# Performance work log

Hardware: AMD Instinct MI355X
Metric: run time of the kernel (lower is better)

Reference implementation:

```python
import jax, jax.numpy as jnp
import numpy as np

B, S, H = 256, 196, 1024  # batch, image_size**2, hidden_size


def _linear_init(key, fan_in, fan_out):
    kw, kb = jax.random.split(key)
    lim = 1.0 / np.sqrt(fan_in)
    W = jax.random.uniform(kw, (fan_in, fan_out), jnp.float32, -lim, lim)
    b = jax.random.uniform(kb, (fan_out,), jnp.float32, -lim, lim)
    return W, b


def setup_inputs() -> dict:
    key = jax.random.key(0)
    ks = jax.random.split(key, 7)
    v = jax.random.normal(ks[0], (B, S, H), jnp.float32)
    h = jax.random.normal(ks[1], (B, H), jnp.float32)
    W_fc, b_fc = _linear_init(ks[2], H, 2 * H)
    W_v, b_v = _linear_init(ks[3], H, H)
    W_h, b_h = _linear_init(ks[4], H, H)
    W_s, b_s = _linear_init(ks[5], H, H)
    W_z, b_z = _linear_init(ks[6], H, 1)
    return {"v": v, "h": h, "W_fc": W_fc, "b_fc": b_fc, "W_v": W_v, "b_v": b_v,
            "W_h": W_h, "b_h": b_h, "W_s": W_s, "b_s": b_s, "W_z": W_z, "b_z": b_z}


def reference(v, h, W_fc, b_fc, W_v, b_v, W_h, b_h, W_s, b_s, W_z, b_z):
    # Dropout is identity in eval mode.
    hs = jnp.tanh(h[:, None, :] @ W_fc + b_fc)          # (B, 1, 2H)
    h1, s = hs[..., :H], hs[..., H:]                    # each (B, 1, H)
    _v = v @ W_v + b_v                                  # (B, S, H)
    _h = h1 @ W_h + b_h                                 # (B, 1, H)
    _s = s @ W_s + b_s                                  # (B, 1, H)
    z = jnp.tanh(jnp.concatenate([_v, _s], axis=1) + _h)  # (B, S+1, H)
    z = (z @ W_z + b_z)[..., 0]                         # (B, S+1)
    a = jax.nn.softmax(z, axis=1)                       # (B, S+1)
    vc = jnp.concatenate([v, s], axis=1)                # (B, S+1, H)
    c = jnp.sum(a[:, :, None] * vc, axis=1)             # (B, H)
    return a, c
```

## Files before the change

### kernel.cpp

```cpp
#include <hip/hip_runtime.h>
#include <hip/hip_bf16.h>
#include <cstdint>
#include <cstddef>

#define Bb  256
#define Ss  196
#define Hh  1024
#define SP1 197
#define Mm  50176

typedef float  f32x4 __attribute__((ext_vector_type(4)));
typedef short  s16x8 __attribute__((ext_vector_type(8)));
typedef unsigned short u16;
typedef unsigned short u16x8 __attribute__((ext_vector_type(8)));

__device__ __forceinline__ u16 f2b(float f) {
  __hip_bfloat16 b = __float2bfloat16(f);
  u16 r; __builtin_memcpy(&r, &b, 2); return r;
}
__device__ __forceinline__ float b2f(u16 u) {
  return __uint_as_float(((unsigned)u) << 16);
}
__device__ __forceinline__ float ftanh(float x) {
  float ax = fabsf(x);
  float t = __expf(-2.f * ax);
  float r = (1.f - t) * __builtin_amdgcn_rcpf(1.f + t);
  return copysignf(r, x);
}
__device__ __forceinline__ void gload16(const u16* g, u16* l) {
  __builtin_amdgcn_global_load_lds(
      (const __attribute__((address_space(1))) unsigned int*)(const void*)g,
      (__attribute__((address_space(3))) unsigned int*)(void*)l, 16, 0, 0);
}

__device__ __forceinline__ void cvtV_core(int bid, const float* __restrict__ V,
                                          u16* __restrict__ Vb) {
  for (int c = bid * 256 + (int)threadIdx.x; c < Mm * 128; c += 2048 * 256) {
    int m = c >> 7;
    int k8 = (c & 127) << 3;
    f32x4 a = *(const f32x4*)(V + (size_t)m * Hh + k8);
    f32x4 b = *(const f32x4*)(V + (size_t)m * Hh + k8 + 4);
    u16x8 w;
    w[0] = f2b(a.x); w[1] = f2b(a.y); w[2] = f2b(a.z); w[3] = f2b(a.w);
    w[4] = f2b(b.x); w[5] = f2b(b.y); w[6] = f2b(b.z); w[7] = f2b(b.w);
    *(u16x8*)(Vb + (size_t)m * Hh + (k8 ^ ((m & 7) << 3))) = w;
  }
}

__device__ __forceinline__ void transpose_core(int bid, float* sm,
                                               const float* __restrict__ Wv,
                                               u16* __restrict__ WvT) {
  float (*t)[65] = (float(*)[65])sm;
  int k0 = (bid & 15) * 64;
  int n0 = (bid >> 4) * 64;
  int tid = threadIdx.x;
#pragma unroll
  for (int i = 0; i < 16; ++i) {
    int idx = i * 256 + tid;
    int r = idx >> 6, c = idx & 63;
    t[r][c] = Wv[(size_t)(k0 + r) * Hh + n0 + c];
  }
  __syncthreads();
#pragma unroll
  for (int i = 0; i < 16; ++i) {
    int idx = i * 256 + tid;
    int r = idx >> 6, c = idx & 63;
    WvT[(size_t)(n0 + r) * Hh + ((k0 + c) ^ ((r & 7) << 3))] = f2b(t[c][r]);
  }
}

__device__ __forceinline__ void small_gemm_core(int bid, int nct, float* sm,
    const float* __restrict__ X, int ldx,
    const float* __restrict__ W, int ldw,
    const float* __restrict__ bias,
    float* __restrict__ Y, int ldy, int act) {
  int tid = threadIdx.x, lane = tid & 63, w = tid >> 6;
  int ct = bid % nct, bt = bid / nct;
  int col = ct * 64 + lane;
  float acc[16];
#pragma unroll
  for (int b = 0; b < 16; ++b) acc[b] = 0.f;
  int xr = lane >> 2, xc = (lane & 3) * 16;
  for (int kc = 0; kc < 4; ++kc) {
    int kb = w * 256 + kc * 64;
#pragma unroll
    for (int q = 0; q < 4; ++q)
      *(f32x4*)&sm[(w * 16 + xr) * 64 + xc + q * 4] =
          *(const f32x4*)&X[(size_t)(bt * 16 + xr) * ldx + kb + xc + q * 4];
    for (int kl = 0; kl < 64; kl += 4) {
      float w0 = W[(size_t)(kb + kl + 0) * ldw + col];
      float w1 = W[(size_t)(kb + kl + 1) * ldw + col];
      float w2 = W[(size_t)(kb + kl + 2) * ldw + col];
      float w3 = W[(size_t)(kb + kl + 3) * ldw + col];
#pragma unroll
      for (int b = 0; b < 16; ++b) {
        f32x4 x = *(const f32x4*)&sm[(w * 16 + b) * 64 + kl];
        acc[b] += x.x * w0 + x.y * w1 + x.z * w2 + x.w * w3;
      }
    }
  }
#pragma unroll
  for (int b = 0; b < 16; ++b) sm[(w * 16 + b) * 64 + lane] = acc[b];
  __syncthreads();
#pragma unroll
  for (int q = 0; q < 4; ++q) {
    int b = w * 4 + q;
    float s = sm[(0 * 16 + b) * 64 + lane] + sm[(1 * 16 + b) * 64 + lane]
            + sm[(2 * 16 + b) * 64 + lane] + sm[(3 * 16 + b) * 64 + lane]
            + bias[col];
    if (act) s = ftanh(s);
    Y[(size_t)(bt * 16 + b) * ldy + col] = s;
  }
}

__global__ __launch_bounds__(256) void k_pre(const float* __restrict__ v,
                                             u16* __restrict__ Vb,
                                             const float* __restrict__ Wv,
                                             u16* __restrict__ WvT,
                                             const float* __restrict__ h,
                                             const float* __restrict__ Wfc,
                                             const float* __restrict__ bfc,
                                             float* __restrict__ hs,
                                             int pre) {
  __shared__ __align__(16) float sm[64 * 65];
  int bid = blockIdx.x;
  if (bid < 2048) {
    if (pre) cvtV_core(bid, v, Vb);
  } else if (bid < 2304) {
    transpose_core(bid - 2048, sm, Wv, WvT);
  } else {
    small_gemm_core(bid - 2304, 32, sm, h, Hh, Wfc, 2048, bfc, hs, 2048, 1);
  }
}

__global__ __launch_bounds__(256) void k_dual(const float* __restrict__ hs,
                                              const float* __restrict__ Wh,
                                              const float* __restrict__ bh,
                                              const float* __restrict__ Ws_,
                                              const float* __restrict__ bs_,
                                              float* __restrict__ hhp,
                                              float* __restrict__ svp) {
  __shared__ __align__(16) float sm[4 * 16 * 64];
  int bid = blockIdx.x;
  int sel = bid >= 256;
  small_gemm_core(bid - (sel << 8), 16, sm,
                  sel ? hs + 1024 : hs, 2048,
                  sel ? Ws_ : Wh, Hh,
                  sel ? bs_ : bh,
                  sel ? svp : hhp, Hh, 0);
}

#define BK 64
template<int PRE>
__global__ __launch_bounds__(256, PRE ? 2 : 3)
void k_big(const float* __restrict__ V, const u16* __restrict__ Vb,
           const u16* __restrict__ WvT, const float* __restrict__ bv,
           const float* __restrict__ hh, const float* __restrict__ Wz,
           float* __restrict__ zpart) {
  constexpr int LDA_ = PRE ? 64 : 72;
  constexpr int NBUF = PRE ? 2 : 1;
  __shared__ __align__(16) u16 As[NBUF][128 * LDA_];
  __shared__ __align__(16) u16 Bs[NBUF][128 * 64];
  __shared__ float wz_s[128], bv_s[128], hh_s[2][128];
  __shared__ float zred[4][64];

  int bid = blockIdx.x;
  int lin = (bid & 7) * 392 + (bid >> 3);
  int mt = lin >> 3, nt = lin & 7;
  int row0 = mt * 128, n0 = nt * 128;

  int tid = threadIdx.x;
  int lane = tid & 63, wid = tid >> 6;
  int wm = wid >> 1, wn = wid & 1;

  int b0 = row0 / Ss;
  int rsplit = (b0 + 1) * Ss - row0;
  int b1 = (rsplit < 128) ? b0 + 1 : b0;
  if (tid < 128) {
    wz_s[tid] = Wz[n0 + tid];
    bv_s[tid] = bv[n0 + tid];
    hh_s[0][tid] = hh[(size_t)b0 * Hh + n0 + tid];
    hh_s[1][tid] = hh[(size_t)b1 * Hh + n0 + tid];
  }

  f32x4 acc[4][4];
  f32x4 zz = {0.f, 0.f, 0.f, 0.f};
#pragma unroll
  for (int m = 0; m < 4; ++m)
#pragma unroll
    for (int n = 0; n < 4; ++n) acc[m][n] = zz;

  int srow = lane >> 3, scol = (lane & 7) * 8;
  int bxor = (lane & 7) << 3;

  auto stage = [&](int kt, int buf) {
    int k0 = kt * BK;
#pragma unroll
    for (int i = 0; i < 4; ++i) {
      int r = wid * 32 + i * 8;
      gload16(WvT + (size_t)(n0 + r + srow) * Hh + k0 + scol, &Bs[buf][r * 64]);
    }
#pragma unroll
    for (int i = 0; i < 4; ++i) {
      int r = wid * 32 + i * 8;
      gload16(Vb + (size_t)(row0 + r + srow) * Hh + k0 + scol, &As[buf][r * 64]);
    }
  };

  int arow = tid >> 3, acol8 = (tid & 7) * 8;
  const float* Ap = V + (size_t)(row0 + arow) * Hh + acol8;
  f32x4 av[8];
  if constexpr (!PRE) {
#pragma unroll
    for (int j = 0; j < 4; ++j) {
      av[2 * j]     = *(const f32x4*)(Ap + (size_t)j * 32 * Hh);
      av[2 * j + 1] = *(const f32x4*)(Ap + (size_t)j * 32 * Hh + 4);
    }
  }

  if constexpr (PRE) {
    stage(0, 0);
    __syncthreads();
  }
  int cur = 0;

  for (int kt = 0; kt < 16; ++kt) {
    if constexpr (PRE) {
      if (kt < 15) stage(kt + 1, cur ^ 1);
    } else {
      int k0 = kt * BK;
      __syncthreads();
#pragma unroll
      for (int i = 0; i < 4; ++i) {
        int r = wid * 32 + i * 8;
        gload16(WvT + (size_t)(n0 + r + srow) * Hh + k0 + scol, &Bs[0][r * 64]);
      }
#pragma unroll
      for (int j = 0; j < 4; ++j) {
        u16x8 w;
        w[0] = f2b(av[2 * j].x);     w[1] = f2b(av[2 * j].y);
        w[2] = f2b(av[2 * j].z);     w[3] = f2b(av[2 * j].w);
        w[4] = f2b(av[2 * j + 1].x); w[5] = f2b(av[2 * j + 1].y);
        w[6] = f2b(av[2 * j + 1].z); w[7] = f2b(av[2 * j + 1].w);
        *(u16x8*)&As[0][(j * 32 + arow) * LDA_ + acol8] = w;
      }
      if (kt < 15) {
#pragma unroll
        for (int j = 0; j < 4; ++j) {
          av[2 * j]     = *(const f32x4*)(Ap + (size_t)j * 32 * Hh + k0 + BK);
          av[2 * j + 1] = *(const f32x4*)(Ap + (size_t)j * 32 * Hh + k0 + BK + 4);
        }
      }
      __syncthreads();
    }
#pragma unroll
    for (int ks = 0; ks < 2; ++ks) {
      int kk = ks * 32 + (lane >> 4) * 8;
      s16x8 afr[4], bfr[4];
#pragma unroll
      for (int m = 0; m < 4; ++m) {
        int r = wm * 64 + m * 16 + (lane & 15);
        afr[m] = *(const s16x8*)&As[cur][r * LDA_ + (PRE ? (kk ^ bxor) : kk)];
      }
#pragma unroll
      for (int n = 0; n < 4; ++n) {
        int r = wn * 64 + n * 16 + (lane & 15);
        bfr[n] = *(const s16x8*)&Bs[cur][r * 64 + (kk ^ bxor)];
      }
#pragma unroll
      for (int m = 0; m < 4; ++m)
#pragma unroll
        for (int n = 0; n < 4; ++n)
          acc[m][n] = __builtin_amdgcn_mfma_f32_16x16x32_bf16(afr[m], bfr[n], acc[m][n], 0, 0, 0);
    }
    if constexpr (PRE) {
      __syncthreads();
      cur ^= 1;
    }
  }

  int cl = lane & 15, rg = lane >> 4;
  float pz[4][4];
#pragma unroll
  for (int m = 0; m < 4; ++m)
#pragma unroll
    for (int j = 0; j < 4; ++j) pz[m][j] = 0.f;
#pragma unroll
  for (int n = 0; n < 4; ++n) {
    int col = wn * 64 + n * 16 + cl;
    float wzv = wz_s[col], bvv = bv_s[col];
    float h0 = hh_s[0][col], h1 = hh_s[1][col];
#pragma unroll
    for (int m = 0; m < 4; ++m)
#pragma unroll
      for (int j = 0; j < 4; ++j) {
        int r = wm * 64 + m * 16 + rg * 4 + j;
        float hv = (r >= rsplit) ? h1 : h0;
        pz[m][j] += wzv * ftanh(acc[m][n][j] + bvv + hv);
      }
  }
#pragma unroll
  for (int m = 0; m < 4; ++m)
#pragma unroll
    for (int j = 0; j < 4; ++j) {
      float vv = pz[m][j];
      vv += __shfl_xor(vv, 1); vv += __shfl_xor(vv, 2);
      vv += __shfl_xor(vv, 4); vv += __shfl_xor(vv, 8);
      pz[m][j] = vv;
    }
  if (cl == 0) {
#pragma unroll
    for (int m = 0; m < 4; ++m)
#pragma unroll
      for (int j = 0; j < 4; ++j)
        zred[wid][m * 16 + rg * 4 + j] = pz[m][j];
  }
  __syncthreads();
  if (tid < 128) {
    int hhalf = tid >> 6, lr = tid & 63;
    zpart[(size_t)nt * Mm + row0 + tid] =
        zred[hhalf * 2][lr] + zred[hhalf * 2 + 1][lr];
  }
}

__global__ __launch_bounds__(256) void k_softmax(const float* __restrict__ zpart,
                                                 const float* __restrict__ sv,
                                                 const float* __restrict__ hhp,
                                                 const float* __restrict__ Wz,
                                                 const float* __restrict__ bz,
                                                 float* __restrict__ outA) {
  int b = blockIdx.x, tid = threadIdx.x;
  int wid = tid >> 6, lane = tid & 63;
  __shared__ float redm[4], reds[4];
  __shared__ float zSsh;
  {
    int j0 = tid * 4;
    f32x4 s4 = *(const f32x4*)&sv[(size_t)b * Hh + j0];
    f32x4 h4 = *(const f32x4*)&hhp[(size_t)b * Hh + j0];
    f32x4 w4 = *(const f32x4*)&Wz[j0];
    float p = w4.x * ftanh(s4.x + h4.x) + w4.y * ftanh(s4.y + h4.y)
            + w4.z * ftanh(s4.z + h4.z) + w4.w * ftanh(s4.w + h4.w);
#pragma unroll
    for (int d = 1; d < 64; d <<= 1) p += __shfl_xor(p, d);
    if (lane == 0) redm[wid] = p;
    __syncthreads();
    if (tid == 0) zSsh = redm[0] + redm[1] + redm[2] + redm[3] + bz[0];
    __syncthreads();
  }
  float z = -1e30f;
  if (tid < Ss) {
    float s = 0.f;
#pragma unroll
    for (int nt = 0; nt < 8; ++nt) s += zpart[(size_t)nt * Mm + (size_t)b * Ss + tid];
    z = s + bz[0];
  } else if (tid == Ss) {
    z = zSsh;
  }
  float m = z;
#pragma unroll
  for (int d = 1; d < 64; d <<= 1) m = fmaxf(m, __shfl_xor(m, d));
  if (lane == 0) redm[wid] = m;
  __syncthreads();
  m = fmaxf(fmaxf(redm[0], redm[1]), fmaxf(redm[2], redm[3]));
  float e = (tid <= Ss) ? expf(z - m) : 0.f;
  float s = e;
#pragma unroll
  for (int d = 1; d < 64; d <<= 1) s += __shfl_xor(s, d);
  if (lane == 0) reds[wid] = s;
  __syncthreads();
  s = reds[0] + reds[1] + reds[2] + reds[3];
  if (tid <= Ss) outA[(size_t)b * SP1 + tid] = e / s;
}

template<int PRE>
__global__ __launch_bounds__(256) void k_ctx(const float* __restrict__ V,
                                             const u16* __restrict__ Vb,
                                             const float* __restrict__ hs,
                                             const float* __restrict__ A,
                                             float* __restrict__ outC) {
  int b = blockIdx.x >> 2;
  int col = (blockIdx.x & 3) * 256 + threadIdx.x;
  __shared__ float a_s[SP1];
  if (threadIdx.x < SP1) a_s[threadIdx.x] = A[(size_t)b * SP1 + threadIdx.x];
  __syncthreads();
  float acc = a_s[Ss] * hs[(size_t)b * 2048 + 1024 + col];
  if constexpr (PRE) {
    size_t m0 = (size_t)b * Ss;
#pragma unroll 4
    for (int t = 0; t < Ss; ++t) {
      size_t m = m0 + t;
      acc += a_s[t] * b2f(Vb[m * Hh + (col ^ (((int)m & 7) << 3))]);
    }
  } else {
    const float* vb = V + (size_t)b * Ss * Hh + col;
#pragma unroll 4
    for (int t = 0; t < Ss; ++t) acc += a_s[t] * vb[(size_t)t * Hh];
  }
  outC[(size_t)b * Hh + col] = acc;
}

extern "C" void kernel_launch(void* const* d_in, const int* in_sizes, int n_in,
                              void* d_out, int out_size, void* d_ws, size_t ws_size,
                              hipStream_t stream) {
  const float* v   = (const float*)d_in[0];
  const float* h   = (const float*)d_in[1];
  const float* Wfc = (const float*)d_in[2];
  const float* bfc = (const float*)d_in[3];
  const float* Wv  = (const float*)d_in[4];
  const float* bv  = (const float*)d_in[5];
  const float* Wh  = (const float*)d_in[6];
  const float* bh  = (const float*)d_in[7];
  const float* Ws  = (const float*)d_in[8];
  const float* bs  = (const float*)d_in[9];
  const float* Wz  = (const float*)d_in[10];
  const float* bz  = (const float*)d_in[11];
  float* out  = (float*)d_out;
  float* outA = out;
  float* outC = out + (size_t)Bb * SP1;

  float* ws  = (float*)d_ws;
  float* hs  = ws;
  float* hh  = hs + 524288;
  float* sv  = hh + 262144;
  float* zp  = sv + 262144;
  u16*  WvT  = (u16*)(zp + 401408);
  u16*  Vb   = (u16*)((char*)(void*)WvT + 2097152);

  bool pre = ws_size >= 110657536ull;

  k_pre<<<2816, 256, 0, stream>>>(v, Vb, Wv, WvT, h, Wfc, bfc, hs, (int)pre);
  k_dual<<<512, 256, 0, stream>>>(hs, Wh, bh, Ws, bs, hh, sv);
  if (pre) k_big<1><<<3136, 256, 0, stream>>>(v, Vb, WvT, bv, hh, Wz, zp);
  else     k_big<0><<<3136, 256, 0, stream>>>(v, Vb, WvT, bv, hh, Wz, zp);
  k_softmax<<<256, 256, 0, stream>>>(zp, sv, hh, Wz, bz, outA);
  if (pre) k_ctx<1><<<1024, 256, 0, stream>>>(v, Vb, hs, outA, outC);
  else     k_ctx<0><<<1024, 256, 0, stream>>>(v, Vb, hs, outA, outC);
}
```

Measured before the change: 311.5 us.

## Move V swizzle into staging loads, drop GEMM double buffer, widen small GEMMs

The V-to-bf16 conversion now writes an unswizzled layout with 16 elements per thread. The XOR swizzle moves into the k_big staging load addresses, which lets k_ctx read contiguous 4-wide bf16 vectors with one block per batch. k_big drops its LDS double buffer to a single buffer with a sync before and after each load, and raises occupancy to 4 blocks per CU. The small GEMMs handle 32 rows per block instead of 16, halving their block counts but doubling register and LDS use per block. The trade is losing load/compute overlap in the main GEMM in exchange for more resident waves.

```diff
diff --git a/kernel.cpp b/kernel.cpp
--- a/kernel.cpp
+++ b/kernel.cpp
@@ -12,6 +12,7 @@
 typedef float  f32x4 __attribute__((ext_vector_type(4)));
 typedef short  s16x8 __attribute__((ext_vector_type(8)));
 typedef unsigned short u16;
+typedef unsigned short u16x4 __attribute__((ext_vector_type(4)));
 typedef unsigned short u16x8 __attribute__((ext_vector_type(8)));
 
 __device__ __forceinline__ u16 f2b(float f) {
@@ -35,15 +36,21 @@
 
 __device__ __forceinline__ void cvtV_core(int bid, const float* __restrict__ V,
                                           u16* __restrict__ Vb) {
-  for (int c = bid * 256 + (int)threadIdx.x; c < Mm * 128; c += 2048 * 256) {
-    int m = c >> 7;
-    int k8 = (c & 127) << 3;
-    f32x4 a = *(const f32x4*)(V + (size_t)m * Hh + k8);
-    f32x4 b = *(const f32x4*)(V + (size_t)m * Hh + k8 + 4);
-    u16x8 w;
-    w[0] = f2b(a.x); w[1] = f2b(a.y); w[2] = f2b(a.z); w[3] = f2b(a.w);
-    w[4] = f2b(b.x); w[5] = f2b(b.y); w[6] = f2b(b.z); w[7] = f2b(b.w);
-    *(u16x8*)(Vb + (size_t)m * Hh + (k8 ^ ((m & 7) << 3))) = w;
+  for (int c = bid * 256 + (int)threadIdx.x; c < Mm * 64; c += 2048 * 256) {
+    int m = c >> 6;
+    int k16 = (c & 63) << 4;
+    const float* src = V + (size_t)m * Hh + k16;
+    f32x4 a = *(const f32x4*)(src);
+    f32x4 b = *(const f32x4*)(src + 4);
+    f32x4 cc = *(const f32x4*)(src + 8);
+    f32x4 d = *(const f32x4*)(src + 12);
+    u16x8 w0, w1;
+    w0[0] = f2b(a.x); w0[1] = f2b(a.y); w0[2] = f2b(a.z); w0[3] = f2b(a.w);
+    w0[4] = f2b(b.x); w0[5] = f2b(b.y); w0[6] = f2b(b.z); w0[7] = f2b(b.w);
+    w1[0] = f2b(cc.x); w1[1] = f2b(cc.y); w1[2] = f2b(cc.z); w1[3] = f2b(cc.w);
+    w1[4] = f2b(d.x); w1[5] = f2b(d.y); w1[6] = f2b(d.z); w1[7] = f2b(d.w);
+    *(u16x8*)(Vb + (size_t)m * Hh + k16) = w0;
+    *(u16x8*)(Vb + (size_t)m * Hh + k16 + 8) = w1;
   }
 }
 
@@ -77,39 +84,39 @@
   int tid = threadIdx.x, lane = tid & 63, w = tid >> 6;
   int ct = bid % nct, bt = bid / nct;
   int col = ct * 64 + lane;
-  float acc[16];
-#pragma unroll
-  for (int b = 0; b < 16; ++b) acc[b] = 0.f;
-  int xr = lane >> 2, xc = (lane & 3) * 16;
+  float acc[32];
+#pragma unroll
+  for (int b = 0; b < 32; ++b) acc[b] = 0.f;
+  int xr = lane >> 1, xc = (lane & 1) * 32;
   for (int kc = 0; kc < 4; ++kc) {
     int kb = w * 256 + kc * 64;
 #pragma unroll
-    for (int q = 0; q < 4; ++q)
-      *(f32x4*)&sm[(w * 16 + xr) * 64 + xc + q * 4] =
-          *(const f32x4*)&X[(size_t)(bt * 16 + xr) * ldx + kb + xc + q * 4];
+    for (int q = 0; q < 8; ++q)
+      *(f32x4*)&sm[(w * 32 + xr) * 64 + xc + q * 4] =
+          *(const f32x4*)&X[(size_t)(bt * 32 + xr) * ldx + kb + xc + q * 4];
     for (int kl = 0; kl < 64; kl += 4) {
       float w0 = W[(size_t)(kb + kl + 0) * ldw + col];
       float w1 = W[(size_t)(kb + kl + 1) * ldw + col];
       float w2 = W[(size_t)(kb + kl + 2) * ldw + col];
       float w3 = W[(size_t)(kb + kl + 3) * ldw + col];
 #pragma unroll
-      for (int b = 0; b < 16; ++b) {
-        f32x4 x = *(const f32x4*)&sm[(w * 16 + b) * 64 + kl];
+      for (int b = 0; b < 32; ++b) {
+        f32x4 x = *(const f32x4*)&sm[(w * 32 + b) * 64 + kl];
         acc[b] += x.x * w0 + x.y * w1 + x.z * w2 + x.w * w3;
       }
     }
   }
 #pragma unroll
-  for (int b = 0; b < 16; ++b) sm[(w * 16 + b) * 64 + lane] = acc[b];
+  for (int b = 0; b < 32; ++b) sm[(w * 32 + b) * 64 + lane] = acc[b];
   __syncthreads();
 #pragma unroll
-  for (int q = 0; q < 4; ++q) {
-    int b = w * 4 + q;
-    float s = sm[(0 * 16 + b) * 64 + lane] + sm[(1 * 16 + b) * 64 + lane]
-            + sm[(2 * 16 + b) * 64 + lane] + sm[(3 * 16 + b) * 64 + lane]
+  for (int q = 0; q < 8; ++q) {
+    int b = w * 8 + q;
+    float s = sm[(0 * 32 + b) * 64 + lane] + sm[(1 * 32 + b) * 64 + lane]
+            + sm[(2 * 32 + b) * 64 + lane] + sm[(3 * 32 + b) * 64 + lane]
             + bias[col];
     if (act) s = ftanh(s);
-    Y[(size_t)(bt * 16 + b) * ldy + col] = s;
+    Y[(size_t)(bt * 32 + b) * ldy + col] = s;
   }
 }
 
@@ -122,7 +129,7 @@
                                              const float* __restrict__ bfc,
                                              float* __restrict__ hs,
                                              int pre) {
-  __shared__ __align__(16) float sm[64 * 65];
+  __shared__ __align__(16) float sm[4 * 32 * 64];
   int bid = blockIdx.x;
   if (bid < 2048) {
     if (pre) cvtV_core(bid, v, Vb);
@@ -140,10 +147,10 @@
                                               const float* __restrict__ bs_,
                                               float* __restrict__ hhp,
                                               float* __restrict__ svp) {
-  __shared__ __align__(16) float sm[4 * 16 * 64];
+  __shared__ __align__(16) float sm[4 * 32 * 64];
   int bid = blockIdx.x;
-  int sel = bid >= 256;
-  small_gemm_core(bid - (sel << 8), 16, sm,
+  int sel = bid >= 128;
+  small_gemm_core(bid - (sel << 7), 16, sm,
                   sel ? hs + 1024 : hs, 2048,
                   sel ? Ws_ : Wh, Hh,
                   sel ? bs_ : bh,
@@ -152,15 +159,14 @@
 
 #define BK 64
 template<int PRE>
-__global__ __launch_bounds__(256, PRE ? 2 : 3)
+__global__ __launch_bounds__(256, PRE ? 4 : 3)
 void k_big(const float* __restrict__ V, const u16* __restrict__ Vb,
            const u16* __restrict__ WvT, const float* __restrict__ bv,
            const float* __restrict__ hh, const float* __restrict__ Wz,
            float* __restrict__ zpart) {
   constexpr int LDA_ = PRE ? 64 : 72;
-  constexpr int NBUF = PRE ? 2 : 1;
-  __shared__ __align__(16) u16 As[NBUF][128 * LDA_];
-  __shared__ __align__(16) u16 Bs[NBUF][128 * 64];
+  __shared__ __align__(16) u16 As[128 * LDA_];
+  __shared__ __align__(16) u16 Bs[128 * 64];
   __shared__ float wz_s[128], bv_s[128], hh_s[2][128];
   __shared__ float zred[4][64];
 
@@ -191,21 +197,8 @@
     for (int n = 0; n < 4; ++n) acc[m][n] = zz;
 
   int srow = lane >> 3, scol = (lane & 7) * 8;
+  int ascol = scol ^ (srow << 3);
   int bxor = (lane & 7) << 3;
-
-  auto stage = [&](int kt, int buf) {
-    int k0 = kt * BK;
-#pragma unroll
-    for (int i = 0; i < 4; ++i) {
-      int r = wid * 32 + i * 8;
-      gload16(WvT + (size_t)(n0 + r + srow) * Hh + k0 + scol, &Bs[buf][r * 64]);
-    }
-#pragma unroll
-    for (int i = 0; i < 4; ++i) {
-      int r = wid * 32 + i * 8;
-      gload16(Vb + (size_t)(row0 + r + srow) * Hh + k0 + scol, &As[buf][r * 64]);
-    }
-  };
 
   int arow = tid >> 3, acol8 = (tid & 7) * 8;
   const float* Ap = V + (size_t)(row0 + arow) * Hh + acol8;
@@ -218,22 +211,25 @@
     }
   }
 
-  if constexpr (PRE) {
-    stage(0, 0);
-    __syncthreads();
-  }
-  int cur = 0;
-
   for (int kt = 0; kt < 16; ++kt) {
+    int k0 = kt * BK;
+    __syncthreads();
     if constexpr (PRE) {
-      if (kt < 15) stage(kt + 1, cur ^ 1);
-    } else {
-      int k0 = kt * BK;
-      __syncthreads();
 #pragma unroll
       for (int i = 0; i < 4; ++i) {
         int r = wid * 32 + i * 8;
-        gload16(WvT + (size_t)(n0 + r + srow) * Hh + k0 + scol, &Bs[0][r * 64]);
+        gload16(WvT + (size_t)(n0 + r + srow) * Hh + k0 + scol, &Bs[r * 64]);
+      }
+#pragma unroll
+      for (int i = 0; i < 4; ++i) {
+        int r = wid * 32 + i * 8;
+        gload16(Vb + (size_t)(row0 + r + srow) * Hh + k0 + ascol, &As[r * 64]);
+      }
+    } else {
+#pragma unroll
+      for (int i = 0; i < 4; ++i) {
+        int r = wid * 32 + i * 8;
+        gload16(WvT + (size_t)(n0 + r + srow) * Hh + k0 + scol, &Bs[r * 64]);
       }
 #pragma unroll
       for (int j = 0; j < 4; ++j) {
@@ -242,7 +238,7 @@
         w[2] = f2b(av[2 * j].z);     w[3] = f2b(av[2 * j].w);
         w[4] = f2b(av[2 * j + 1].x); w[5] = f2b(av[2 * j + 1].y);
         w[6] = f2b(av[2 * j + 1].z); w[7] = f2b(av[2 * j + 1].w);
-        *(u16x8*)&As[0][(j * 32 + arow) * LDA_ + acol8] = w;
+        *(u16x8*)&As[(j * 32 + arow) * LDA_ + acol8] = w;
       }
       if (kt < 15) {
 #pragma unroll
@@ -251,8 +247,8 @@
           av[2 * j + 1] = *(const f32x4*)(Ap + (size_t)j * 32 * Hh + k0 + BK + 4);
         }
       }
-      __syncthreads();
-    }
+    }
+    __syncthreads();
 #pragma unroll
     for (int ks = 0; ks < 2; ++ks) {
       int kk = ks * 32 + (lane >> 4) * 8;
@@ -260,22 +256,18 @@
 #pragma unroll
       for (int m = 0; m < 4; ++m) {
         int r = wm * 64 + m * 16 + (lane & 15);
-        afr[m] = *(const s16x8*)&As[cur][r * LDA_ + (PRE ? (kk ^ bxor) : kk)];
+        afr[m] = *(const s16x8*)&As[r * LDA_ + (PRE ? (kk ^ bxor) : kk)];
       }
 #pragma unroll
       for (int n = 0; n < 4; ++n) {
         int r = wn * 64 + n * 16 + (lane & 15);
-        bfr[n] = *(const s16x8*)&Bs[cur][r * 64 + (kk ^ bxor)];
+        bfr[n] = *(const s16x8*)&Bs[r * 64 + (kk ^ bxor)];
       }
 #pragma unroll
       for (int m = 0; m < 4; ++m)
 #pragma unroll
         for (int n = 0; n < 4; ++n)
           acc[m][n] = __builtin_amdgcn_mfma_f32_16x16x32_bf16(afr[m], bfr[n], acc[m][n], 0, 0, 0);
-    }
-    if constexpr (PRE) {
-      __syncthreads();
-      cur ^= 1;
     }
   }
 
@@ -378,25 +370,35 @@
                                              const float* __restrict__ hs,
                                              const float* __restrict__ A,
                                              float* __restrict__ outC) {
-  int b = blockIdx.x >> 2;
-  int col = (blockIdx.x & 3) * 256 + threadIdx.x;
   __shared__ float a_s[SP1];
-  if (threadIdx.x < SP1) a_s[threadIdx.x] = A[(size_t)b * SP1 + threadIdx.x];
-  __syncthreads();
-  float acc = a_s[Ss] * hs[(size_t)b * 2048 + 1024 + col];
   if constexpr (PRE) {
-    size_t m0 = (size_t)b * Ss;
+    int b = blockIdx.x;
+    int c4 = threadIdx.x * 4;
+    if (threadIdx.x < SP1) a_s[threadIdx.x] = A[(size_t)b * SP1 + threadIdx.x];
+    __syncthreads();
+    f32x4 hv = *(const f32x4*)&hs[(size_t)b * 2048 + 1024 + c4];
+    float aS = a_s[Ss];
+    f32x4 acc = {aS * hv.x, aS * hv.y, aS * hv.z, aS * hv.w};
+    const u16* vb = Vb + (size_t)b * Ss * Hh + c4;
 #pragma unroll 4
     for (int t = 0; t < Ss; ++t) {
-      size_t m = m0 + t;
-      acc += a_s[t] * b2f(Vb[m * Hh + (col ^ (((int)m & 7) << 3))]);
-    }
+      u16x4 w = *(const u16x4*)(vb + (size_t)t * Hh);
+      float at = a_s[t];
+      acc.x += at * b2f(w[0]); acc.y += at * b2f(w[1]);
+      acc.z += at * b2f(w[2]); acc.w += at * b2f(w[3]);
+    }
+    *(f32x4*)&outC[(size_t)b * Hh + c4] = acc;
   } else {
+    int b = blockIdx.x >> 2;
+    int col = (blockIdx.x & 3) * 256 + threadIdx.x;
+    if (threadIdx.x < SP1) a_s[threadIdx.x] = A[(size_t)b * SP1 + threadIdx.x];
+    __syncthreads();
+    float acc = a_s[Ss] * hs[(size_t)b * 2048 + 1024 + col];
     const float* vb = V + (size_t)b * Ss * Hh + col;
 #pragma unroll 4
     for (int t = 0; t < Ss; ++t) acc += a_s[t] * vb[(size_t)t * Hh];
-  }
-  outC[(size_t)b * Hh + col] = acc;
+    outC[(size_t)b * Hh + col] = acc;
+  }
 }
 
 extern "C" void kernel_launch(void* const* d_in, const int* in_sizes, int n_in,
@@ -428,11 +430,11 @@
 
   bool pre = ws_size >= 110657536ull;
 
-  k_pre<<<2816, 256, 0, stream>>>(v, Vb, Wv, WvT, h, Wfc, bfc, hs, (int)pre);
-  k_dual<<<512, 256, 0, stream>>>(hs, Wh, bh, Ws, bs, hh, sv);
+  k_pre<<<2560, 256, 0, stream>>>(v, Vb, Wv, WvT, h, Wfc, bfc, hs, (int)pre);
+  k_dual<<<256, 256, 0, stream>>>(hs, Wh, bh, Ws, bs, hh, sv);
   if (pre) k_big<1><<<3136, 256, 0, stream>>>(v, Vb, WvT, bv, hh, Wz, zp);
   else     k_big<0><<<3136, 256, 0, stream>>>(v, Vb, WvT, bv, hh, Wz, zp);
   k_softmax<<<256, 256, 0, stream>>>(zp, sv, hh, Wz, bz, outA);
-  if (pre) k_ctx<1><<<1024, 256, 0, stream>>>(v, Vb, hs, outA, outC);
+  if (pre) k_ctx<1><<<256, 256, 0, stream>>>(v, Vb, hs, outA, outC);
   else     k_ctx<0><<<1024, 256, 0, stream>>>(v, Vb, hs, outA, outC);
 }
```

Result: slower. 367.2 us (+17.9%).
